# Performance work log

Hardware: AMD Instinct MI355X
Metric: run time of the kernel (lower is better)

## Reference

```python
import jax, jax.numpy as jnp
import numpy as np

HEADS = 8
BN_EPS = 1e-5

def _bn(x2d, g, b):
    # torch BatchNorm1d in training mode: biased batch stats
    mu = x2d.mean(0)
    var = x2d.var(0)
    return (x2d - mu) * jax.lax.rsqrt(var + BN_EPS) * g + b

def _window_indices(H):
    # exclusive-end box coordinates, in the exact order of the torch loop
    m = H // 2
    r0, r1, c0, c1 = [], [], [], []
    for i in range(1, m + 1):
        wins = [(m - i, m + i + 1, m - i, m + i + 1),  # full square
                (m - i, m + 1,     m - i, m + i + 1),  # top half
                (m,     m + i + 1, m - i, m + i + 1),  # bottom half
                (m - i, m + i + 1, m - i, m + 1),      # left half
                (m - i, m + i + 1, m,     m + i + 1)]  # right half
        for a, b, c, d in wins:
            r0.append(a); r1.append(b); c0.append(c); c1.append(d)
    r0 = np.array(r0); r1 = np.array(r1); c0 = np.array(c0); c1 = np.array(c1)
    counts = ((r1 - r0) * (c1 - c0)).astype(np.float32)
    return r0, r1, c0, c1, counts

def _box_sums(P, r0, r1, c0, c1):
    # P: padded 2D prefix sum [B, C, H+1, H+1]; returns [B, C, K]
    return P[:, :, r1, c1] - P[:, :, r0, c1] - P[:, :, r1, c0] + P[:, :, r0, c0]

def _integral(img):
    return jnp.pad(jnp.cumsum(jnp.cumsum(img, axis=2), axis=3), ((0, 0), (0, 0), (1, 0), (1, 0)))

def setup_inputs() -> dict:
    key = jax.random.key(0)
    ks = jax.random.split(key, 8)
    B, Cin, H = 64, 512, 31
    C = 512  # heads * base_dim
    x = jax.random.normal(ks[0], (B, Cin, H, H), dtype=jnp.float32)
    w_v = jax.random.normal(ks[1], (Cin, C), dtype=jnp.float32) * 0.02
    w_k = jax.random.normal(ks[2], (Cin, C), dtype=jnp.float32) * 0.02
    w_fc = jax.random.normal(ks[3], (Cin + C, 512), dtype=jnp.float32) * 0.02
    z = lambda n: jnp.zeros((n,), jnp.float32)
    o = lambda n: jnp.ones((n,), jnp.float32)
    return {"x": x,
            "w_v": w_v, "b_v": z(C), "g_vn": o(C), "b_vn": z(C),
            "w_k": w_k, "b_k": z(C), "g_kn": o(C), "b_kn": z(C),
            "w_fc": w_fc, "b_fc": z(512), "g_fcn": o(512), "b_fcn": z(512)}

def reference(x, w_v, b_v, g_vn, b_vn, w_k, b_k, g_kn, b_kn, w_fc, b_fc, g_fcn, b_fcn):
    B, Cin, H, W = x.shape
    N = H * W
    C = w_v.shape[1]
    d = C // HEADS
    m = H // 2
    xt = x.reshape(B, Cin, N).transpose(0, 2, 1)       # [B, N, Cin]
    x0 = xt[:, N // 2, :]                              # [B, Cin] center pixel feature
    flat = xt.reshape(B * N, Cin)
    v = jax.nn.relu(_bn(flat @ w_v + b_v, g_vn, b_vn))
    v = v.reshape(B, N, C).transpose(0, 2, 1).reshape(B, C, H, H)
    k = _bn(flat @ w_k + b_k, g_kn, b_kn).reshape(B, N, HEADS, d).transpose(0, 2, 1, 3)  # [B,h,N,d]
    q = k[:, :, N // 2, :]                             # [B, h, d]
    attn = jax.nn.softmax(jnp.einsum('bhd,bhnd->bhn', q, k) * (d ** -0.5), axis=-1)      # [B,h,N]
    attn_full = jnp.broadcast_to(attn[:, :, None, :], (B, HEADS, d, N)).reshape(B, C, H, H)
    xw = attn_full * v                                 # attn-weighted values [B,C,H,H]
    eps = 1e-16
    r0, r1, c0, c1, counts = _window_indices(H)
    Px = _integral(xw)
    Pa = _integral(attn_full)
    mx = _box_sums(Px, r0, r1, c0, c1) / counts        # window means of xw   [B,C,K]
    ma = _box_sums(Pa, r0, r1, c0, c1) / counts        # window means of attn [B,C,K]
    y_win = (mx / (ma + eps)).transpose(0, 2, 1)       # [B, K, C]
    y = jnp.concatenate([xw[:, :, m, m][:, None, :], y_win], axis=1)  # [B, n, C]
    # F.normalize(p=2, dim=2)
    y = y / jnp.maximum(jnp.linalg.norm(y, axis=2, keepdims=True), 1e-12)
    n = y.shape[1]
    yy = jnp.concatenate([jnp.broadcast_to(x0[:, None, :], (B, n, Cin)), y], axis=-1)
    out = jax.nn.relu(_bn(yy.reshape(B * n, Cin + C) @ w_fc + b_fc, g_fcn, b_fcn))
    return out.reshape(B, n, -1)
```

## Files before the change

### kernel.cpp

```cpp
#include <hip/hip_runtime.h>
#include <stdint.h>

#define DEV __device__ __forceinline__

typedef __bf16 bf16x8 __attribute__((ext_vector_type(8)));
typedef unsigned short u16x8 __attribute__((ext_vector_type(8)));
typedef float f32x4 __attribute__((ext_vector_type(4)));

#define NS 992

DEV uint16_t f2bf(float f) {
    union { float f; uint32_t u; } v; v.f = f;
    uint32_t r = v.u + 0x7fffu + ((v.u >> 16) & 1u);
    return (uint16_t)(r >> 16);
}
DEV float bf2f(uint16_t h) {
    union { uint32_t u; float f; } v; v.u = ((uint32_t)h) << 16;
    return v.f;
}
DEV float bflo(uint32_t w) { union { uint32_t u; float f; } v; v.u = w << 16; return v.f; }
DEV float bfhi(uint32_t w) { union { uint32_t u; float f; } v; v.u = w & 0xffff0000u; return v.f; }

#if __has_builtin(__builtin_amdgcn_cvt_pk_bf16_f32)
typedef __bf16 bf16x2 __attribute__((ext_vector_type(2)));
DEV uint32_t pk2bf(float lo, float hi) {
    bf16x2 r = __builtin_amdgcn_cvt_pk_bf16_f32(lo, hi);
    return __builtin_bit_cast(uint32_t, r);
}
#else
DEV uint32_t pk2bf(float lo, float hi) {
    return (uint32_t)f2bf(lo) | ((uint32_t)f2bf(hi) << 16);
}
#endif

DEV float scan32(float v, int lane) {
    #pragma unroll
    for (int d = 1; d < 32; d <<= 1) {
        float o = __shfl_up(v, d, 32);
        if (lane >= d) v += o;
    }
    return v;
}

#if __has_builtin(__builtin_amdgcn_global_load_lds)
DEV void async16(const uint16_t* g, uint16_t* l) {
    __builtin_amdgcn_global_load_lds(
        (const __attribute__((address_space(1))) uint32_t*)g,
        (__attribute__((address_space(3))) uint32_t*)l, 16, 0, 0);
}
#else
DEV void async16(const uint16_t* g, uint16_t* l) {
    *(u16x8*)l = *(const u16x8*)g;
}
#endif

__global__ void k_convert_x(const float* __restrict__ x, uint16_t* __restrict__ xbt) {
    __shared__ float tile[32][33];
    int b = blockIdx.z;
    int n0 = blockIdx.x * 32;
    int c0 = blockIdx.y * 32;
    int tx = threadIdx.x, ty = threadIdx.y;
    #pragma unroll
    for (int i = 0; i < 4; ++i) {
        int c = c0 + ty + 8 * i;
        int n = n0 + tx;
        float v = 0.f;
        if (n < 961) v = x[((size_t)b * 512 + c) * 961 + n];
        tile[ty + 8 * i][tx] = v;
    }
    __syncthreads();
    int idx = ty * 32 + tx;
    int c4 = (idx & 7) * 4;
    int nl = idx >> 3;
    int n = n0 + nl;
    ushort4 val;
    val.x = f2bf(tile[c4 + 0][nl]);
    val.y = f2bf(tile[c4 + 1][nl]);
    val.z = f2bf(tile[c4 + 2][nl]);
    val.w = f2bf(tile[c4 + 3][nl]);
    *(ushort4*)&xbt[((size_t)b * NS + n) * 512 + c0 + c4] = val;
}

__global__ void k_convert_w(const float* __restrict__ wv, const float* __restrict__ wk,
                            const float* __restrict__ wfc,
                            uint16_t* __restrict__ wvkt, uint16_t* __restrict__ wfct) {
    int idx = blockIdx.x * 256 + threadIdx.x;
    if (idx < 524288) {
        int j = idx >> 9, k = idx & 511;
        float v = (j < 512) ? wv[(size_t)k * 512 + j] : wk[(size_t)k * 512 + (j - 512)];
        wvkt[idx] = f2bf(v);
    } else {
        int t = idx - 524288;
        int j = t >> 10, k = t & 1023;
        wfct[t] = f2bf(wfc[(size_t)k * 512 + j]);
    }
}

template<int K, int EPI>
__global__ __launch_bounds__(256, 4)
void k_gemm(const uint16_t* __restrict__ A, const uint16_t* __restrict__ Bt,
            uint16_t* __restrict__ out_v, uint16_t* __restrict__ out_k,
            float* __restrict__ out_f,
            float* __restrict__ colsum, float* __restrict__ colsq)
{
    __shared__ __align__(16) uint16_t sbuf[16384];
    __shared__ float sStat[256];
    uint16_t* sA0 = sbuf;
    uint16_t* sA1 = sbuf + 4096;
    uint16_t* sB0 = sbuf + 8192;
    uint16_t* sB1 = sbuf + 12288;

    const int tid = threadIdx.x;
    const int wave = tid >> 6, lane = tid & 63;
    const int quad = lane >> 4, l16 = lane & 15;
    int m0, j0;
    if constexpr (EPI == 0) {
        int lin = blockIdx.x;
        int xcd = lin & 7, rest = lin >> 3;
        int jb = rest & 7, mhi = rest >> 3;
        m0 = (mhi * 8 + xcd) * 128; j0 = jb * 128;
    } else {
        m0 = blockIdx.y * 128; j0 = blockIdx.x * 128;
    }
    const int wm = wave >> 1, wj = wave & 1;

    const f32x4 fzero = {0.f, 0.f, 0.f, 0.f};
    f32x4 acc[4][4];
    #pragma unroll
    for (int i = 0; i < 4; ++i)
        #pragma unroll
        for (int j = 0; j < 4; ++j) acc[i][j] = fzero;

    const int c0 = tid;
    const int mA0 = c0 >> 2, kq0 = c0 & 3;
    const int c1 = tid + 256;
    const int mA1 = c1 >> 2, kq1 = c1 & 3;

    const int KT = K / 64;
    for (int kt = 0; kt < KT; ++kt) {
        const uint16_t* Ak = A + (size_t)m0 * K + kt * 64;
        const uint16_t* Bk = Bt + (size_t)j0 * K + kt * 64;
        async16(Ak + (size_t)mA0 * K + kq0 * 8,      &sA0[c0 * 8]);
        async16(Ak + (size_t)mA1 * K + kq1 * 8,      &sA0[c1 * 8]);
        async16(Ak + (size_t)mA0 * K + 32 + kq0 * 8, &sA1[c0 * 8]);
        async16(Ak + (size_t)mA1 * K + 32 + kq1 * 8, &sA1[c1 * 8]);
        async16(Bk + (size_t)mA0 * K + kq0 * 8,      &sB0[c0 * 8]);
        async16(Bk + (size_t)mA1 * K + kq1 * 8,      &sB0[c1 * 8]);
        async16(Bk + (size_t)mA0 * K + 32 + kq0 * 8, &sB1[c0 * 8]);
        async16(Bk + (size_t)mA1 * K + 32 + kq1 * 8, &sB1[c1 * 8]);
        __syncthreads();
        #pragma unroll
        for (int p = 0; p < 2; ++p) {
            const uint16_t* pA = p ? sA1 : sA0;
            const uint16_t* pB = p ? sB1 : sB0;
            bf16x8 af[4], bfr[4];
            #pragma unroll
            for (int i = 0; i < 4; ++i) {
                int m = wm * 64 + i * 16 + l16;
                u16x8 r = *(const u16x8*)&pA[m * 32 + quad * 8];
                af[i] = __builtin_bit_cast(bf16x8, r);
            }
            #pragma unroll
            for (int j = 0; j < 4; ++j) {
                int jj = wj * 64 + j * 16 + l16;
                u16x8 r = *(const u16x8*)&pB[jj * 32 + quad * 8];
                bfr[j] = __builtin_bit_cast(bf16x8, r);
            }
            #pragma unroll
            for (int i = 0; i < 4; ++i)
                #pragma unroll
                for (int j = 0; j < 4; ++j)
                    acc[i][j] = __builtin_amdgcn_mfma_f32_16x16x32_bf16(af[i], bfr[j], acc[i][j], 0, 0, 0);
        }
        __syncthreads();
    }

    sStat[tid] = 0.f;
    __syncthreads();

    #pragma unroll
    for (int j = 0; j < 4; ++j) {
        const int col_local = wj * 64 + j * 16 + l16;
        float ls = 0.f, lq = 0.f;
        #pragma unroll
        for (int i = 0; i < 4; ++i) {
            #pragma unroll
            for (int reg = 0; reg < 4; ++reg) {
                const float val = acc[i][j][reg];
                ls += val; lq += val * val;
                if constexpr (EPI == 1) {
                    const int r = m0 + wm * 64 + i * 16 + quad * 4 + reg;
                    out_f[(size_t)r * 512 + (j0 + col_local)] = val;
                }
            }
        }
        ls += __shfl_xor(ls, 16); lq += __shfl_xor(lq, 16);
        ls += __shfl_xor(ls, 32); lq += __shfl_xor(lq, 32);
        if (quad == 0) {
            atomicAdd(&sStat[col_local], ls);
            atomicAdd(&sStat[128 + col_local], lq);
        }
    }
    __syncthreads();
    if (tid < 128) atomicAdd(&colsum[j0 + tid], sStat[tid]);
    else           atomicAdd(&colsq[j0 + (tid & 127)], sStat[tid]);

    if constexpr (EPI == 0) {
        #pragma unroll
        for (int ch = 0; ch < 2; ++ch) {
            if (wj == ch) {
                #pragma unroll
                for (int j = 0; j < 4; ++j) {
                    const int c = j * 16 + l16;
                    #pragma unroll
                    for (int i = 0; i < 4; ++i) {
                        const int rloc = wm * 64 + i * 16 + quad * 4;
                        uint2 pp;
                        pp.x = pk2bf(acc[i][j][0], acc[i][j][1]);
                        pp.y = pk2bf(acc[i][j][2], acc[i][j][3]);
                        *(uint2*)&sbuf[c * 136 + rloc] = pp;
                    }
                }
            }
            __syncthreads();
            const int jg = j0 + ch * 64;
            uint16_t* const outp = (jg < 512) ? out_v : out_k;
            const int jbase = (jg < 512) ? jg : jg - 512;
            #pragma unroll
            for (int s = 0; s < 8; ++s) {
                const int chunk = tid + 256 * s;
                const int c = chunk >> 5, q = chunk & 31;
                uint2 val = *(const uint2*)&sbuf[c * 136 + q * 4];
                const int r = m0 + q * 4;
                const unsigned bb_ = (unsigned)r / (unsigned)NS;
                const unsigned nn = (unsigned)r - bb_ * (unsigned)NS;
                *(uint2*)&outp[((size_t)bb_ * 512 + jbase + c) * NS + nn] = val;
            }
            __syncthreads();
        }
    }
}

__global__ void k_attn(const uint16_t* __restrict__ kraw,
                       const float* __restrict__ colsum, const float* __restrict__ colsq,
                       const float* __restrict__ g_kn, const float* __restrict__ b_kn,
                       float* __restrict__ attn, float* __restrict__ maw)
{
    __shared__ float qa[64];
    __shared__ float s_qb;
    __shared__ float att[961];
    __shared__ float red[8];

    int bh = blockIdx.x;
    int b = bh >> 3, h = bh & 7;
    int tid = threadIdx.x;
    constexpr float invM = 1.f / 61504.f;

    if (tid < 64) {
        int c = h * 64 + tid;
        float mean = colsum[512 + c] * invM;
        float q_ = colsq[512 + c] * invM;
        float a = g_kn[c] * rsqrtf(q_ - mean * mean + 1e-5f);
        float bb = b_kn[c] - mean * a;
        float kr = bf2f(kraw[((size_t)b * 512 + c) * NS + 480]);
        float qv = kr * a + bb;
        qa[tid] = qv * a;
        float qb = qv * bb;
        for (int off = 32; off; off >>= 1) qb += __shfl_down(qb, off);
        if (tid == 0) s_qb = qb;
    }
    __syncthreads();

    const int n4 = tid * 4;
    const bool active = n4 < 961;
    float a0 = 0.f, a1 = 0.f, a2 = 0.f, a3 = 0.f;
    if (active) {
        const uint16_t* kp = kraw + ((size_t)b * 512 + h * 64) * NS + n4;
        #pragma unroll 16
        for (int dd = 0; dd < 64; ++dd) {
            uint2 kk = *(const uint2*)(kp + (size_t)dd * NS);
            float q = qa[dd];
            a0 += q * bflo(kk.x);
            a1 += q * bfhi(kk.x);
            a2 += q * bflo(kk.y);
            a3 += q * bfhi(kk.y);
        }
    }
    float lg[4] = {a0, a1, a2, a3};
    float lmax = -1e30f;
    #pragma unroll
    for (int i = 0; i < 4; ++i) {
        lg[i] = (lg[i] + s_qb) * 0.125f;
        if (n4 + i < 961) lmax = fmaxf(lmax, lg[i]);
    }
    for (int off = 32; off; off >>= 1) lmax = fmaxf(lmax, __shfl_xor(lmax, off));
    if ((tid & 63) == 0) red[tid >> 6] = lmax;
    __syncthreads();
    float bmax = fmaxf(fmaxf(red[0], red[1]), fmaxf(red[2], red[3]));

    float lsum = 0.f;
    #pragma unroll
    for (int i = 0; i < 4; ++i) {
        float e = (n4 + i < 961) ? __expf(lg[i] - bmax) : 0.f;
        lg[i] = e;
        lsum += e;
    }
    for (int off = 32; off; off >>= 1) lsum += __shfl_xor(lsum, off);
    if ((tid & 63) == 0) red[4 + (tid >> 6)] = lsum;
    __syncthreads();
    float inv = 1.f / (red[4] + red[5] + red[6] + red[7]);
    if (active) {
        f32x4 v = {lg[0] * inv, lg[1] * inv, lg[2] * inv, lg[3] * inv};
        if (n4 <= 956) { *(f32x4*)&att[n4] = v; }
        else { att[956] = v[0]; att[957] = v[1]; att[958] = v[2]; att[959] = v[3]; att[960] = lg[0]; }
        if (n4 == 956) att[960] = v[0] * 0.f + lg[0] * 0.f;
        *(f32x4*)&attn[(size_t)bh * NS + n4] = v;
    }
    if (tid == 240) att[960] = lg[0] * inv;
    __syncthreads();

    {
        int r8 = tid >> 5, col = tid & 31;
        #pragma unroll
        for (int p = 0; p < 4; ++p) {
            int row = p * 8 + r8;
            bool on = (row < 31) && (col < 31);
            float v = on ? att[row * 31 + col] : 0.f;
            v = scan32(v, col);
            if (on) att[row * 31 + col] = v;
        }
    }
    __syncthreads();
    {
        int c8 = tid >> 5, r = tid & 31;
        #pragma unroll
        for (int p = 0; p < 4; ++p) {
            int c = p * 8 + c8;
            bool on = (c < 31) && (r < 31);
            float v = on ? att[r * 31 + c] : 0.f;
            v = scan32(v, r);
            if (on) att[r * 31 + c] = v;
        }
    }
    __syncthreads();

    if (tid < 75) {
        int i = tid / 5 + 1, t = tid % 5;
        const int m = 15;
        int r0, r1, cc0, cc1;
        switch (t) {
            case 0: r0 = m - i; r1 = m + i + 1; cc0 = m - i; cc1 = m + i + 1; break;
            case 1: r0 = m - i; r1 = m + 1;     cc0 = m - i; cc1 = m + i + 1; break;
            case 2: r0 = m;     r1 = m + i + 1; cc0 = m - i; cc1 = m + i + 1; break;
            case 3: r0 = m - i; r1 = m + i + 1; cc0 = m - i; cc1 = m + 1;     break;
            default:r0 = m - i; r1 = m + i + 1; cc0 = m;     cc1 = m + i + 1; break;
        }
        auto S = [&](int r, int c) -> float { return (r < 0 || c < 0) ? 0.f : att[r * 31 + c]; };
        float box = S(r1 - 1, cc1 - 1) - S(r0 - 1, cc1 - 1) - S(r1 - 1, cc0 - 1) + S(r0 - 1, cc0 - 1);
        float cnt = (float)((r1 - r0) * (cc1 - cc0));
        maw[(size_t)bh * 75 + tid] = box / cnt;
    }
}

__global__ void k_winbox(const uint16_t* __restrict__ vraw,
                         const float* __restrict__ colsum, const float* __restrict__ colsq,
                         const float* __restrict__ g_vn, const float* __restrict__ b_vn,
                         const float* __restrict__ attn, const float* __restrict__ maw,
                         float* __restrict__ y)
{
    __shared__ float xw[961];
    __shared__ float s_center;
    int bc = blockIdx.x;
    int b = bc >> 9, c = bc & 511;
    int h = c >> 6;
    int tid = threadIdx.x;
    constexpr float invM = 1.f / 61504.f;
    float mean = colsum[c] * invM;
    float q_ = colsq[c] * invM;
    float a = g_vn[c] * rsqrtf(q_ - mean * mean + 1e-5f);
    float bb = b_vn[c] - mean * a;
    const uint16_t* vp = vraw + (size_t)bc * NS;
    const float* ap = attn + (size_t)(b * 8 + h) * NS;
    int n4 = tid * 4;
    if (n4 < 961) {
        uint2 kk = *(const uint2*)(vp + n4);
        f32x4 at = *(const f32x4*)(ap + n4);
        f32x4 v;
        v[0] = fmaxf(bflo(kk.x) * a + bb, 0.f) * at[0];
        v[1] = fmaxf(bfhi(kk.x) * a + bb, 0.f) * at[1];
        v[2] = fmaxf(bflo(kk.y) * a + bb, 0.f) * at[2];
        v[3] = fmaxf(bfhi(kk.y) * a + bb, 0.f) * at[3];
        if (n4 <= 956) { *(f32x4*)&xw[n4] = v; }
        else { xw[956] = v[0]; xw[957] = v[1]; xw[958] = v[2]; xw[959] = v[3]; }
        if (n4 == 960) xw[960] = v[0];
    }
    __syncthreads();
    if (tid == 0) s_center = xw[480];
    __syncthreads();
    {
        int r8 = tid >> 5, col = tid & 31;
        #pragma unroll
        for (int p = 0; p < 4; ++p) {
            int row = p * 8 + r8;
            bool on = (row < 31) && (col < 31);
            float v = on ? xw[row * 31 + col] : 0.f;
            v = scan32(v, col);
            if (on) xw[row * 31 + col] = v;
        }
    }
    __syncthreads();
    {
        int c8 = tid >> 5, r = tid & 31;
        #pragma unroll
        for (int p = 0; p < 4; ++p) {
            int cc = p * 8 + c8;
            bool on = (cc < 31) && (r < 31);
            float v = on ? xw[r * 31 + cc] : 0.f;
            v = scan32(v, r);
            if (on) xw[r * 31 + cc] = v;
        }
    }
    __syncthreads();
    if (tid < 75) {
        int i = tid / 5 + 1, t = tid % 5;
        const int m = 15;
        int r0, r1, cc0, cc1;
        switch (t) {
            case 0: r0 = m - i; r1 = m + i + 1; cc0 = m - i; cc1 = m + i + 1; break;
            case 1: r0 = m - i; r1 = m + 1;     cc0 = m - i; cc1 = m + i + 1; break;
            case 2: r0 = m;     r1 = m + i + 1; cc0 = m - i; cc1 = m + i + 1; break;
            case 3: r0 = m - i; r1 = m + i + 1; cc0 = m - i; cc1 = m + 1;     break;
            default:r0 = m - i; r1 = m + i + 1; cc0 = m;     cc1 = m + i + 1; break;
        }
        auto S = [&](int r, int cc) -> float { return (r < 0 || cc < 0) ? 0.f : xw[r * 31 + cc]; };
        float box = S(r1 - 1, cc1 - 1) - S(r0 - 1, cc1 - 1) - S(r1 - 1, cc0 - 1) + S(r0 - 1, cc0 - 1);
        float cnt = (float)((r1 - r0) * (cc1 - cc0));
        float mx = box / cnt;
        float ma = maw[(size_t)(b * 8 + h) * 75 + tid];
        y[((size_t)b * 76 + 1 + tid) * 512 + c] = mx / (ma + 1e-16f);
    }
    if (tid == 96) y[((size_t)b * 76) * 512 + c] = s_center;
}

__global__ void k_build_yy(const float* __restrict__ y, const uint16_t* __restrict__ xbt,
                           uint16_t* __restrict__ yy)
{
    __shared__ float red[4];
    int row = blockIdx.x;
    int b = row / 76;
    int tid = threadIdx.x;
    const float* yp = y + (size_t)row * 512;
    float v0 = yp[tid], v1 = yp[tid + 256];
    float ss = v0 * v0 + v1 * v1;
    for (int off = 32; off; off >>= 1) ss += __shfl_xor(ss, off);
    if ((tid & 63) == 0) red[tid >> 6] = ss;
    __syncthreads();
    float tot = red[0] + red[1] + red[2] + red[3];
    float inv = 1.f / fmaxf(sqrtf(tot), 1e-12f);
    uint16_t* op = yy + (size_t)row * 1024;
    const uint16_t* x0p = xbt + ((size_t)b * NS + 480) * 512;
    op[tid]           = x0p[tid];
    op[tid + 256]     = x0p[tid + 256];
    op[512 + tid]       = f2bf(v0 * inv);
    op[512 + tid + 256] = f2bf(v1 * inv);
}

__global__ void k_fcout(const float* __restrict__ fcraw,
                        const float* __restrict__ colsum, const float* __restrict__ colsq,
                        const float* __restrict__ g, const float* __restrict__ be,
                        float* __restrict__ out)
{
    size_t idx = (size_t)blockIdx.x * 256 + threadIdx.x;
    if (idx < (size_t)4864 * 512) {
        int j = (int)(idx & 511);
        constexpr float invM = 1.f / 4864.f;
        float mean = colsum[j] * invM;
        float q_ = colsq[j] * invM;
        float a = g[j] * rsqrtf(q_ - mean * mean + 1e-5f);
        float bb = be[j] - mean * a;
        out[idx] = fmaxf(fcraw[idx] * a + bb, 0.f);
    }
}

extern "C" void kernel_launch(void* const* d_in, const int* in_sizes, int n_in,
                              void* d_out, int out_size, void* d_ws, size_t ws_size,
                              hipStream_t stream)
{
    (void)in_sizes; (void)n_in; (void)out_size; (void)ws_size;
    const float* x    = (const float*)d_in[0];
    const float* w_v  = (const float*)d_in[1];
    const float* g_vn = (const float*)d_in[3];
    const float* b_vn = (const float*)d_in[4];
    const float* w_k  = (const float*)d_in[5];
    const float* g_kn = (const float*)d_in[7];
    const float* b_kn = (const float*)d_in[8];
    const float* w_fc = (const float*)d_in[9];
    const float* g_fcn = (const float*)d_in[11];
    const float* b_fcn = (const float*)d_in[12];
    float* out = (float*)d_out;

    char* base = (char*)d_ws;
    size_t off = 0;
    auto alloc = [&](size_t bytes) -> void* {
        void* p = base + off;
        off += (bytes + 255) & ~(size_t)255;
        return p;
    };
    uint16_t* xbt  = (uint16_t*)alloc((size_t)64 * NS * 512 * 2);
    uint16_t* wvkt = (uint16_t*)alloc((size_t)1024 * 512 * 2);
    uint16_t* wfct = (uint16_t*)alloc((size_t)512 * 1024 * 2);
    uint16_t* vraw = (uint16_t*)alloc((size_t)64 * 512 * NS * 2);
    uint16_t* kraw = (uint16_t*)alloc((size_t)64 * 512 * NS * 2);
    float* stats   = (float*)alloc(3072 * 4);
    float* attn    = (float*)alloc((size_t)512 * NS * 4);
    float* maw     = (float*)alloc((size_t)512 * 75 * 4);
    float* y       = (float*)alloc((size_t)64 * 76 * 512 * 4);
    uint16_t* yy   = (uint16_t*)alloc((size_t)4864 * 1024 * 2);
    float* fcraw   = (float*)alloc((size_t)4864 * 512 * 4);

    hipMemsetAsync(stats, 0, 3072 * 4, stream);
    k_convert_x<<<dim3(31, 16, 64), dim3(32, 8), 0, stream>>>(x, xbt);
    k_convert_w<<<4096, 256, 0, stream>>>(w_v, w_k, w_fc, wvkt, wfct);

    k_gemm<512, 0><<<3968, 256, 0, stream>>>(xbt, wvkt, vraw, kraw, nullptr,
                                             stats, stats + 1024);

    k_attn<<<512, 256, 0, stream>>>(kraw, stats, stats + 1024, g_kn, b_kn, attn, maw);
    k_winbox<<<64 * 512, 256, 0, stream>>>(vraw, stats, stats + 1024, g_vn, b_vn, attn, maw, y);
    k_build_yy<<<4864, 256, 0, stream>>>(y, xbt, yy);

    k_gemm<1024, 1><<<dim3(4, 38), 256, 0, stream>>>(yy, wfct, nullptr, nullptr, fcraw,
                                                     stats + 2048, stats + 2560);
    k_fcout<<<9728, 256, 0, stream>>>(fcraw, stats + 2048, stats + 2560, g_fcn, b_fcn, out);
}
```

Baseline: 451.8 us.

## Fuse attention softmax and windowed box-sum kernels into one per-head kernel

Merges k_attn and k_winbox into a single 1024-thread kernel per (batch, head). It computes the softmax in LDS and then loops over the head's 64 channels four at a time, doing the 2D prefix scans and window box sums in place. This drops the global attn/maw round trip and one launch. The trade is that the 32768-block winbox grid shrinks to 512 blocks with serial channel loops and many barriers, which risks low occupancy and parallelism.

```diff
diff --git a/kernel.cpp b/kernel.cpp
--- a/kernel.cpp
+++ b/kernel.cpp
@@ -40,6 +40,18 @@
         if (lane >= d) v += o;
     }
     return v;
+}
+
+DEV void win_idx(int w, int& r0, int& r1, int& c0, int& c1) {
+    int i = w / 5 + 1, t = w % 5;
+    const int m = 15;
+    switch (t) {
+        case 0: r0 = m - i; r1 = m + i + 1; c0 = m - i; c1 = m + i + 1; break;
+        case 1: r0 = m - i; r1 = m + 1;     c0 = m - i; c1 = m + i + 1; break;
+        case 2: r0 = m;     r1 = m + i + 1; c0 = m - i; c1 = m + i + 1; break;
+        case 3: r0 = m - i; r1 = m + i + 1; c0 = m - i; c1 = m + 1;     break;
+        default:r0 = m - i; r1 = m + i + 1; c0 = m;     c1 = m + i + 1; break;
+    }
 }
 
 #if __has_builtin(__builtin_amdgcn_global_load_lds)
@@ -241,19 +253,24 @@
     }
 }
 
-__global__ void k_attn(const uint16_t* __restrict__ kraw,
-                       const float* __restrict__ colsum, const float* __restrict__ colsq,
-                       const float* __restrict__ g_kn, const float* __restrict__ b_kn,
-                       float* __restrict__ attn, float* __restrict__ maw)
+__global__ __launch_bounds__(1024, 2)
+void k_attnwin(const uint16_t* __restrict__ kraw, const uint16_t* __restrict__ vraw,
+               const float* __restrict__ colsum, const float* __restrict__ colsq,
+               const float* __restrict__ g_kn, const float* __restrict__ b_kn,
+               const float* __restrict__ g_vn, const float* __restrict__ b_vn,
+               float* __restrict__ y)
 {
     __shared__ float qa[64];
-    __shared__ float s_qb;
-    __shared__ float att[961];
-    __shared__ float red[8];
-
-    int bh = blockIdx.x;
-    int b = bh >> 3, h = bh & 7;
-    int tid = threadIdx.x;
+    __shared__ float va[64], vb[64];
+    __shared__ float atv[964];
+    __shared__ float xw[4][964];
+    __shared__ float maw_s[76];
+    __shared__ float red[16];
+    __shared__ float s_qb, s_bmax, s_inv;
+
+    const int bh = blockIdx.x;
+    const int b = bh >> 3, h = bh & 7;
+    const int tid = threadIdx.x;
     constexpr float invM = 1.f / 61504.f;
 
     if (tid < 64) {
@@ -266,180 +283,146 @@
         float qv = kr * a + bb;
         qa[tid] = qv * a;
         float qb = qv * bb;
+        #pragma unroll
         for (int off = 32; off; off >>= 1) qb += __shfl_down(qb, off);
         if (tid == 0) s_qb = qb;
-    }
-    __syncthreads();
-
-    const int n4 = tid * 4;
-    const bool active = n4 < 961;
-    float a0 = 0.f, a1 = 0.f, a2 = 0.f, a3 = 0.f;
-    if (active) {
-        const uint16_t* kp = kraw + ((size_t)b * 512 + h * 64) * NS + n4;
+    } else if (tid >= 64 && tid < 128) {
+        int t = tid - 64;
+        int c = h * 64 + t;
+        float mean = colsum[c] * invM;
+        float q_ = colsq[c] * invM;
+        float a = g_vn[c] * rsqrtf(q_ - mean * mean + 1e-5f);
+        va[t] = a;
+        vb[t] = b_vn[c] - mean * a;
+    }
+    __syncthreads();
+
+    float lg = -1e30f;
+    if (tid < 961) {
+        const uint16_t* kp = kraw + ((size_t)b * 512 + h * 64) * NS + tid;
+        float acc = 0.f;
         #pragma unroll 16
-        for (int dd = 0; dd < 64; ++dd) {
-            uint2 kk = *(const uint2*)(kp + (size_t)dd * NS);
-            float q = qa[dd];
-            a0 += q * bflo(kk.x);
-            a1 += q * bfhi(kk.x);
-            a2 += q * bflo(kk.y);
-            a3 += q * bfhi(kk.y);
-        }
-    }
-    float lg[4] = {a0, a1, a2, a3};
-    float lmax = -1e30f;
+        for (int dd = 0; dd < 64; ++dd)
+            acc += qa[dd] * bf2f(kp[(size_t)dd * NS]);
+        lg = (acc + s_qb) * 0.125f;
+    }
+    float lmax = lg;
     #pragma unroll
-    for (int i = 0; i < 4; ++i) {
-        lg[i] = (lg[i] + s_qb) * 0.125f;
-        if (n4 + i < 961) lmax = fmaxf(lmax, lg[i]);
-    }
     for (int off = 32; off; off >>= 1) lmax = fmaxf(lmax, __shfl_xor(lmax, off));
     if ((tid & 63) == 0) red[tid >> 6] = lmax;
     __syncthreads();
-    float bmax = fmaxf(fmaxf(red[0], red[1]), fmaxf(red[2], red[3]));
-
-    float lsum = 0.f;
+    if (tid < 64) {
+        float v = (tid < 16) ? red[tid] : -1e30f;
+        #pragma unroll
+        for (int off = 8; off; off >>= 1) v = fmaxf(v, __shfl_xor(v, off));
+        if (tid == 0) s_bmax = v;
+    }
+    __syncthreads();
+    float e = (tid < 961) ? __expf(lg - s_bmax) : 0.f;
+    float lsum = e;
     #pragma unroll
-    for (int i = 0; i < 4; ++i) {
-        float e = (n4 + i < 961) ? __expf(lg[i] - bmax) : 0.f;
-        lg[i] = e;
-        lsum += e;
-    }
     for (int off = 32; off; off >>= 1) lsum += __shfl_xor(lsum, off);
-    if ((tid & 63) == 0) red[4 + (tid >> 6)] = lsum;
-    __syncthreads();
-    float inv = 1.f / (red[4] + red[5] + red[6] + red[7]);
-    if (active) {
-        f32x4 v = {lg[0] * inv, lg[1] * inv, lg[2] * inv, lg[3] * inv};
-        if (n4 <= 956) { *(f32x4*)&att[n4] = v; }
-        else { att[956] = v[0]; att[957] = v[1]; att[958] = v[2]; att[959] = v[3]; att[960] = lg[0]; }
-        if (n4 == 956) att[960] = v[0] * 0.f + lg[0] * 0.f;
-        *(f32x4*)&attn[(size_t)bh * NS + n4] = v;
-    }
-    if (tid == 240) att[960] = lg[0] * inv;
+    if ((tid & 63) == 0) red[tid >> 6] = lsum;
+    __syncthreads();
+    if (tid < 64) {
+        float v = (tid < 16) ? red[tid] : 0.f;
+        #pragma unroll
+        for (int off = 8; off; off >>= 1) v += __shfl_xor(v, off);
+        if (tid == 0) s_inv = 1.f / v;
+    }
+    __syncthreads();
+    if (tid < 961) {
+        float a = e * s_inv;
+        atv[tid] = a;
+        xw[0][tid] = a;
+    }
     __syncthreads();
 
     {
-        int r8 = tid >> 5, col = tid & 31;
-        #pragma unroll
-        for (int p = 0; p < 4; ++p) {
-            int row = p * 8 + r8;
-            bool on = (row < 31) && (col < 31);
-            float v = on ? att[row * 31 + col] : 0.f;
-            v = scan32(v, col);
-            if (on) att[row * 31 + col] = v;
-        }
+        int row = tid >> 5, col = tid & 31;
+        bool on = (tid < 992) && (col < 31);
+        float v = on ? xw[0][row * 31 + col] : 0.f;
+        v = scan32(v, col);
+        if (on) xw[0][row * 31 + col] = v;
     }
     __syncthreads();
     {
-        int c8 = tid >> 5, r = tid & 31;
-        #pragma unroll
-        for (int p = 0; p < 4; ++p) {
-            int c = p * 8 + c8;
-            bool on = (c < 31) && (r < 31);
-            float v = on ? att[r * 31 + c] : 0.f;
-            v = scan32(v, r);
-            if (on) att[r * 31 + c] = v;
-        }
-    }
-    __syncthreads();
-
+        int cc = tid >> 5, r = tid & 31;
+        bool on = (tid < 992) && (r < 31);
+        float v = on ? xw[0][r * 31 + cc] : 0.f;
+        v = scan32(v, r);
+        if (on) xw[0][r * 31 + cc] = v;
+    }
+    __syncthreads();
     if (tid < 75) {
-        int i = tid / 5 + 1, t = tid % 5;
-        const int m = 15;
-        int r0, r1, cc0, cc1;
-        switch (t) {
-            case 0: r0 = m - i; r1 = m + i + 1; cc0 = m - i; cc1 = m + i + 1; break;
-            case 1: r0 = m - i; r1 = m + 1;     cc0 = m - i; cc1 = m + i + 1; break;
-            case 2: r0 = m;     r1 = m + i + 1; cc0 = m - i; cc1 = m + i + 1; break;
-            case 3: r0 = m - i; r1 = m + i + 1; cc0 = m - i; cc1 = m + 1;     break;
-            default:r0 = m - i; r1 = m + i + 1; cc0 = m;     cc1 = m + i + 1; break;
-        }
-        auto S = [&](int r, int c) -> float { return (r < 0 || c < 0) ? 0.f : att[r * 31 + c]; };
-        float box = S(r1 - 1, cc1 - 1) - S(r0 - 1, cc1 - 1) - S(r1 - 1, cc0 - 1) + S(r0 - 1, cc0 - 1);
-        float cnt = (float)((r1 - r0) * (cc1 - cc0));
-        maw[(size_t)bh * 75 + tid] = box / cnt;
-    }
-}
-
-__global__ void k_winbox(const uint16_t* __restrict__ vraw,
-                         const float* __restrict__ colsum, const float* __restrict__ colsq,
-                         const float* __restrict__ g_vn, const float* __restrict__ b_vn,
-                         const float* __restrict__ attn, const float* __restrict__ maw,
-                         float* __restrict__ y)
-{
-    __shared__ float xw[961];
-    __shared__ float s_center;
-    int bc = blockIdx.x;
-    int b = bc >> 9, c = bc & 511;
-    int h = c >> 6;
-    int tid = threadIdx.x;
-    constexpr float invM = 1.f / 61504.f;
-    float mean = colsum[c] * invM;
-    float q_ = colsq[c] * invM;
-    float a = g_vn[c] * rsqrtf(q_ - mean * mean + 1e-5f);
-    float bb = b_vn[c] - mean * a;
-    const uint16_t* vp = vraw + (size_t)bc * NS;
-    const float* ap = attn + (size_t)(b * 8 + h) * NS;
-    int n4 = tid * 4;
-    if (n4 < 961) {
-        uint2 kk = *(const uint2*)(vp + n4);
-        f32x4 at = *(const f32x4*)(ap + n4);
-        f32x4 v;
-        v[0] = fmaxf(bflo(kk.x) * a + bb, 0.f) * at[0];
-        v[1] = fmaxf(bfhi(kk.x) * a + bb, 0.f) * at[1];
-        v[2] = fmaxf(bflo(kk.y) * a + bb, 0.f) * at[2];
-        v[3] = fmaxf(bfhi(kk.y) * a + bb, 0.f) * at[3];
-        if (n4 <= 956) { *(f32x4*)&xw[n4] = v; }
-        else { xw[956] = v[0]; xw[957] = v[1]; xw[958] = v[2]; xw[959] = v[3]; }
-        if (n4 == 960) xw[960] = v[0];
-    }
-    __syncthreads();
-    if (tid == 0) s_center = xw[480];
-    __syncthreads();
-    {
-        int r8 = tid >> 5, col = tid & 31;
-        #pragma unroll
-        for (int p = 0; p < 4; ++p) {
-            int row = p * 8 + r8;
-            bool on = (row < 31) && (col < 31);
-            float v = on ? xw[row * 31 + col] : 0.f;
-            v = scan32(v, col);
-            if (on) xw[row * 31 + col] = v;
-        }
-    }
-    __syncthreads();
-    {
-        int c8 = tid >> 5, r = tid & 31;
-        #pragma unroll
-        for (int p = 0; p < 4; ++p) {
-            int cc = p * 8 + c8;
-            bool on = (cc < 31) && (r < 31);
-            float v = on ? xw[r * 31 + cc] : 0.f;
-            v = scan32(v, r);
-            if (on) xw[r * 31 + cc] = v;
-        }
-    }
-    __syncthreads();
-    if (tid < 75) {
-        int i = tid / 5 + 1, t = tid % 5;
-        const int m = 15;
-        int r0, r1, cc0, cc1;
-        switch (t) {
-            case 0: r0 = m - i; r1 = m + i + 1; cc0 = m - i; cc1 = m + i + 1; break;
-            case 1: r0 = m - i; r1 = m + 1;     cc0 = m - i; cc1 = m + i + 1; break;
-            case 2: r0 = m;     r1 = m + i + 1; cc0 = m - i; cc1 = m + i + 1; break;
-            case 3: r0 = m - i; r1 = m + i + 1; cc0 = m - i; cc1 = m + 1;     break;
-            default:r0 = m - i; r1 = m + i + 1; cc0 = m;     cc1 = m + i + 1; break;
-        }
-        auto S = [&](int r, int cc) -> float { return (r < 0 || cc < 0) ? 0.f : xw[r * 31 + cc]; };
-        float box = S(r1 - 1, cc1 - 1) - S(r0 - 1, cc1 - 1) - S(r1 - 1, cc0 - 1) + S(r0 - 1, cc0 - 1);
-        float cnt = (float)((r1 - r0) * (cc1 - cc0));
-        float mx = box / cnt;
-        float ma = maw[(size_t)(b * 8 + h) * 75 + tid];
-        y[((size_t)b * 76 + 1 + tid) * 512 + c] = mx / (ma + 1e-16f);
-    }
-    if (tid == 96) y[((size_t)b * 76) * 512 + c] = s_center;
+        int r0, r1, c0, c1;
+        win_idx(tid, r0, r1, c0, c1);
+        auto S = [&](int r, int c) -> float { return (r < 0 || c < 0) ? 0.f : xw[0][r * 31 + c]; };
+        float box = S(r1 - 1, c1 - 1) - S(r0 - 1, c1 - 1) - S(r1 - 1, c0 - 1) + S(r0 - 1, c0 - 1);
+        float cnt = (float)((r1 - r0) * (c1 - c0));
+        maw_s[tid] = box / cnt;
+    }
+    __syncthreads();
+
+    const uint16_t* vbase = vraw + ((size_t)b * 512 + h * 64) * NS + tid;
+    float pv[4];
+    if (tid < 961) {
+        #pragma unroll
+        for (int u = 0; u < 4; ++u) pv[u] = bf2f(vbase[(size_t)u * NS]);
+    }
+    for (int cp = 0; cp < 16; ++cp) {
+        if (tid < 961) {
+            float myatt = atv[tid];
+            #pragma unroll
+            for (int u = 0; u < 4; ++u) {
+                int cl = cp * 4 + u;
+                float w = fmaxf(pv[u] * va[cl] + vb[cl], 0.f) * myatt;
+                xw[u][tid] = w;
+                if (tid == 480) y[(size_t)b * 76 * 512 + (h * 64 + cl)] = w;
+            }
+            if (cp < 15) {
+                #pragma unroll
+                for (int u = 0; u < 4; ++u) pv[u] = bf2f(vbase[(size_t)(cp * 4 + 4 + u) * NS]);
+            }
+        }
+        __syncthreads();
+        {
+            int row = tid >> 5, col = tid & 31;
+            bool on = (tid < 992) && (col < 31);
+            #pragma unroll
+            for (int u = 0; u < 4; ++u) {
+                float v = on ? xw[u][row * 31 + col] : 0.f;
+                v = scan32(v, col);
+                if (on) xw[u][row * 31 + col] = v;
+            }
+        }
+        __syncthreads();
+        {
+            int cc = tid >> 5, r = tid & 31;
+            bool on = (tid < 992) && (r < 31);
+            #pragma unroll
+            for (int u = 0; u < 4; ++u) {
+                float v = on ? xw[u][r * 31 + cc] : 0.f;
+                v = scan32(v, r);
+                if (on) xw[u][r * 31 + cc] = v;
+            }
+        }
+        __syncthreads();
+        {
+            int u = tid >> 8, w = tid & 255;
+            if (w < 75) {
+                int r0, r1, c0, c1;
+                win_idx(w, r0, r1, c0, c1);
+                auto S = [&](int r, int c) -> float { return (r < 0 || c < 0) ? 0.f : xw[u][r * 31 + c]; };
+                float box = S(r1 - 1, c1 - 1) - S(r0 - 1, c1 - 1) - S(r1 - 1, c0 - 1) + S(r0 - 1, c0 - 1);
+                float cnt = (float)((r1 - r0) * (c1 - c0));
+                float mx = box / cnt;
+                int cl = cp * 4 + u;
+                y[((size_t)b * 76 + 1 + w) * 512 + (h * 64 + cl)] = mx / (maw_s[w] + 1e-16f);
+            }
+        }
+        __syncthreads();
+    }
 }
 
 __global__ void k_build_yy(const float* __restrict__ y, const uint16_t* __restrict__ xbt,
@@ -512,8 +495,6 @@
     uint16_t* vraw = (uint16_t*)alloc((size_t)64 * 512 * NS * 2);
     uint16_t* kraw = (uint16_t*)alloc((size_t)64 * 512 * NS * 2);
     float* stats   = (float*)alloc(3072 * 4);
-    float* attn    = (float*)alloc((size_t)512 * NS * 4);
-    float* maw     = (float*)alloc((size_t)512 * 75 * 4);
     float* y       = (float*)alloc((size_t)64 * 76 * 512 * 4);
     uint16_t* yy   = (uint16_t*)alloc((size_t)4864 * 1024 * 2);
     float* fcraw   = (float*)alloc((size_t)4864 * 512 * 4);
@@ -525,8 +506,8 @@
     k_gemm<512, 0><<<3968, 256, 0, stream>>>(xbt, wvkt, vraw, kraw, nullptr,
                                              stats, stats + 1024);
 
-    k_attn<<<512, 256, 0, stream>>>(kraw, stats, stats + 1024, g_kn, b_kn, attn, maw);
-    k_winbox<<<64 * 512, 256, 0, stream>>>(vraw, stats, stats + 1024, g_vn, b_vn, attn, maw, y);
+    k_attnwin<<<512, 1024, 0, stream>>>(kraw, vraw, stats, stats + 1024,
+                                        g_kn, b_kn, g_vn, b_vn, y);
     k_build_yy<<<4864, 256, 0, stream>>>(y, xbt, yy);
 
     k_gemm<1024, 1><<<dim3(4, 38), 256, 0, stream>>>(yy, wfct, nullptr, nullptr, fcraw,
```

Result: slower. 462.7 us (+2.4%).
